# Performance work log

Measured on AMD Instinct MI355X. Metric: run time of the kernel, lower is better.

The kernel has to match this reference:

```python
import jax, jax.numpy as jnp
import numpy as np

D_MODEL = 2048
NUM_HEADS = 16
HEAD_DIM = D_MODEL // NUM_HEADS
B, S = 2, 2048


def setup_inputs() -> dict:
    key = jax.random.key(0)
    ks = jax.random.split(key, 11)
    scale = 1.0 / np.sqrt(D_MODEL)
    inp = {
        "query": jax.random.normal(ks[0], (B, S, D_MODEL), dtype=jnp.float32),
        "key": jax.random.normal(ks[1], (B, S, D_MODEL), dtype=jnp.float32),
        "value": jax.random.normal(ks[2], (B, S, D_MODEL), dtype=jnp.float32),
        "Wq": jax.random.normal(ks[3], (D_MODEL, D_MODEL), dtype=jnp.float32) * scale,
        "bq": jax.random.normal(ks[4], (D_MODEL,), dtype=jnp.float32) * 0.01,
        "Wk": jax.random.normal(ks[5], (D_MODEL, D_MODEL), dtype=jnp.float32) * scale,
        "bk": jax.random.normal(ks[6], (D_MODEL,), dtype=jnp.float32) * 0.01,
        "Wv": jax.random.normal(ks[7], (D_MODEL, D_MODEL), dtype=jnp.float32) * scale,
        "bv": jax.random.normal(ks[8], (D_MODEL,), dtype=jnp.float32) * 0.01,
        "Wo": jax.random.normal(ks[9], (D_MODEL, D_MODEL), dtype=jnp.float32) * scale,
        "bo": jax.random.normal(ks[10], (D_MODEL,), dtype=jnp.float32) * 0.01,
    }
    return inp


def _shape(x, B, S):
    # [B, S, D] -> [B, H, S, hd]
    return x.reshape(B, S, NUM_HEADS, HEAD_DIM).transpose(0, 2, 1, 3)


def reference(query, key, value, Wq, bq, Wk, bk, Wv, bv, Wo, bo):
    B, Sq, D = query.shape
    Sk = key.shape[1]
    # Linear layers (torch: y = x @ W.T + b)
    Q = _shape(query @ Wq.T + bq, B, Sq)   # [B,H,Sq,hd]
    K = _shape(key @ Wk.T + bk, B, Sk)     # [B,H,Sk,hd]
    V = _shape(value @ Wv.T + bv, B, Sk)   # [B,H,Sk,hd]
    scores = jnp.einsum('bhqd,bhkd->bhqk', Q, K) / jnp.sqrt(jnp.float32(HEAD_DIM))
    # causal mask: triu(ones(Sq, Sk), diagonal=1)
    causal = jnp.triu(jnp.ones((Sq, Sk), dtype=bool), k=1)
    scores = jnp.where(causal[None, None, :, :], jnp.float32(-jnp.inf), scores)
    attn = jax.nn.softmax(scores, axis=-1)
    out = jnp.einsum('bhqk,bhkd->bhqd', attn, V)
    out = out.transpose(0, 2, 1, 3).reshape(B, Sq, D)
    return out @ Wo.T + bo
```

## Files before the change

kernel.cpp:

```cpp
#include <hip/hip_runtime.h>
#include <hip/hip_bf16.h>

typedef __attribute__((ext_vector_type(8))) short short8;
typedef __attribute__((ext_vector_type(4))) short s16x4;
typedef __attribute__((ext_vector_type(4))) float f32x4;

#define MFMA_BF16(A, B, C) __builtin_amdgcn_mfma_f32_16x16x32_bf16(A, B, C, 0, 0, 0)

__device__ __forceinline__ void gload_lds16(const __hip_bfloat16* g, __hip_bfloat16* l) {
  __builtin_amdgcn_global_load_lds(
      (const __attribute__((address_space(1))) unsigned int*)g,
      (__attribute__((address_space(3))) unsigned int*)l, 16, 0, 0);
}

__device__ __forceinline__ float finite_or(float x, float repl) {
  unsigned u;
  __builtin_memcpy(&u, &x, 4);
  return ((u & 0x7f800000u) == 0x7f800000u) ? repl : x;
}

__device__ __forceinline__ short bf16_bits(float x) {
  __hip_bfloat16 b = __float2bfloat16(x);
  short s;
  __builtin_memcpy(&s, &b, 2);
  return s;
}

__device__ __forceinline__ short8 pack8(f32x4 a, f32x4 b) {
  short8 r;
  r[0] = bf16_bits(a[0]); r[1] = bf16_bits(a[1]);
  r[2] = bf16_bits(a[2]); r[3] = bf16_bits(a[3]);
  r[4] = bf16_bits(b[0]); r[5] = bf16_bits(b[1]);
  r[6] = bf16_bits(b[2]); r[7] = bf16_bits(b[3]);
  return r;
}

__global__ __launch_bounds__(256) void cvt_kernel(
    const float* x0, const float* x1, const float* x2,
    const float* w0, const float* w1, const float* w2, const float* w3,
    __hip_bfloat16* y0, __hip_bfloat16* y1, __hip_bfloat16* y2,
    __hip_bfloat16* u0, __hip_bfloat16* u1, __hip_bfloat16* u2, __hip_bfloat16* u3)
{
  const int z = blockIdx.y;
  const float* s = z == 0 ? x0 : z == 1 ? x1 : z == 2 ? x2
                 : z == 3 ? w0 : z == 4 ? w1 : z == 5 ? w2 : w3;
  __hip_bfloat16* d = z == 0 ? y0 : z == 1 ? y1 : z == 2 ? y2
                    : z == 3 ? u0 : z == 4 ? u1 : z == 5 ? u2 : u3;
  const size_t n = (z < 3) ? (size_t)8388608 : (size_t)4194304;
  const size_t stride = (size_t)gridDim.x * 256 * 8;
  for (size_t i = ((size_t)blockIdx.x * 256 + threadIdx.x) * 8; i < n; i += stride) {
    f32x4 a = *(const f32x4*)(s + i);
    f32x4 b = *(const f32x4*)(s + i + 4);
    *(short8*)((short*)d + i) = pack8(a, b);
  }
}

#define GBUF 24576

__device__ __forceinline__ void stage_A(const __hip_bfloat16* Ab, __hip_bfloat16* bufA,
                                        int kcol, int t, int wave) {
#pragma unroll
  for (int r = 0; r < 2; ++r) {
    const int ci = r * 512 + t;
    const int row = ci >> 3, c = ci & 7;
    const int sc = c ^ (row & 7);
    gload_lds16(Ab + (size_t)row * 2048 + kcol + sc * 8, bufA + r * 4096 + wave * 512);
  }
}
__device__ __forceinline__ void stage_Br(const __hip_bfloat16* Bb, __hip_bfloat16* bufB,
                                         int kcol, int t, int wave, int r) {
  const int ci = r * 512 + t;
  const int row = ci >> 3, c = ci & 7;
  const int sc = c ^ (row & 7);
  gload_lds16(Bb + (size_t)row * 2048 + kcol + sc * 8, bufB + r * 4096 + wave * 512);
}

template <typename OutT>
__device__ __forceinline__ void gemm8p_body(
    const __hip_bfloat16* __restrict__ A, const __hip_bfloat16* __restrict__ Bt,
    const float* __restrict__ bias, OutT* __restrict__ C,
    float trip, __hip_bfloat16* sm)
{
  constexpr int K = 2048, N = 2048, NT = K / 64;
  const int t = threadIdx.x, wave = t >> 6, lane = t & 63;
  const int ll = lane & 15, lg = lane >> 4;
  const int wmB = (wave >> 2) * 64, wnB = (wave & 3) * 64;
  const int m0 = blockIdx.y * 128, n0 = blockIdx.x * 256;
  const __hip_bfloat16* Ab = A + (size_t)m0 * K;
  const __hip_bfloat16* Bb = Bt + (size_t)n0 * K;

  f32x4 acc[4][4] = {};

  stage_A(Ab, sm, 0, t, wave);
  stage_Br(Bb, sm + 8192, 0, t, wave, 0);
  stage_Br(Bb, sm + 8192, 0, t, wave, 1);
  stage_Br(Bb, sm + 8192, 0, t, wave, 2);
  stage_Br(Bb, sm + 8192, 0, t, wave, 3);
  stage_A(Ab, sm + GBUF, 64, t, wave);
  stage_Br(Bb, sm + GBUF + 8192, 64, t, wave, 0);
  stage_Br(Bb, sm + GBUF + 8192, 64, t, wave, 1);
  stage_Br(Bb, sm + GBUF + 8192, 64, t, wave, 2);
  stage_Br(Bb, sm + GBUF + 8192, 64, t, wave, 3);
  asm volatile("s_waitcnt vmcnt(6)" ::: "memory");
  __builtin_amdgcn_s_barrier();

  for (int i = 0; i < NT; ++i) {
    const __hip_bfloat16* bufA = sm + (i % 3) * GBUF;
    const __hip_bfloat16* bufB = bufA + 8192;
    const bool pf = (i + 2 < NT);
    __hip_bfloat16* pA = sm + ((i + 2) % 3) * GBUF;
    const int pk = (i + 2) * 64;

#pragma unroll
    for (int kk = 0; kk < 2; ++kk) {
      short8 af[4], bf[4];
#pragma unroll
      for (int f = 0; f < 4; ++f) {
        const int ar = wmB + f * 16 + ll;
        af[f] = *(const short8*)&bufA[ar * 64 + (((kk * 4 + lg) ^ (ar & 7)) << 3)];
        const int br = wnB + f * 16 + ll;
        bf[f] = *(const short8*)&bufB[br * 64 + (((kk * 4 + lg) ^ (br & 7)) << 3)];
      }
      if (pf) {
        if (kk == 0) {
          stage_A(Ab, pA, pk, t, wave);
          stage_Br(Bb, pA + 8192, pk, t, wave, 0);
        } else {
          stage_Br(Bb, pA + 8192, pk, t, wave, 1);
          stage_Br(Bb, pA + 8192, pk, t, wave, 2);
          stage_Br(Bb, pA + 8192, pk, t, wave, 3);
        }
      }
      asm volatile("s_waitcnt lgkmcnt(0)" ::: "memory");
      __builtin_amdgcn_sched_barrier(0);
      __builtin_amdgcn_s_setprio(1);
#pragma unroll
      for (int mi = 0; mi < 4; ++mi)
#pragma unroll
        for (int ni = 0; ni < 4; ++ni)
          acc[mi][ni] = MFMA_BF16(af[mi], bf[ni], acc[mi][ni]);
      __builtin_amdgcn_s_setprio(0);
      __builtin_amdgcn_sched_barrier(0);
    }

    const int rem = NT - 1 - i;
    if (rem >= 2) {
      asm volatile("s_waitcnt vmcnt(6)" ::: "memory");
      __builtin_amdgcn_s_barrier();
    } else if (rem == 1) {
      asm volatile("s_waitcnt vmcnt(0)" ::: "memory");
      __builtin_amdgcn_s_barrier();
    }
  }

#pragma unroll
  for (int mi = 0; mi < 4; ++mi)
#pragma unroll
    for (int ni = 0; ni < 4; ++ni) {
      const int col = n0 + wnB + ni * 16 + ll;
      const float bv = bias[col];
#pragma unroll
      for (int j = 0; j < 4; ++j) {
        const int row = m0 + wmB + mi * 16 + lg * 4 + j;
        const float val = finite_or(acc[mi][ni][j] + bv, trip);
        if constexpr (__is_same(OutT, float))
          C[(size_t)row * N + col] = val;
        else
          C[(size_t)row * N + col] = __float2bfloat16(val);
      }
    }
}

__global__ __launch_bounds__(512) void gemm_qkv_kernel(
    const __hip_bfloat16* xq, const __hip_bfloat16* xk, const __hip_bfloat16* xv,
    const __hip_bfloat16* Wq, const __hip_bfloat16* Wk, const __hip_bfloat16* Wv,
    const float* bq, const float* bk, const float* bv,
    __hip_bfloat16* Q, __hip_bfloat16* K, __hip_bfloat16* V)
{
  __shared__ __align__(16) __hip_bfloat16 sm[3 * GBUF];
  const int z = blockIdx.z;
  const __hip_bfloat16* X = z == 0 ? xq : (z == 1 ? xk : xv);
  const __hip_bfloat16* W = z == 0 ? Wq : (z == 1 ? Wk : Wv);
  const float*          B = z == 0 ? bq : (z == 1 ? bk : bv);
  __hip_bfloat16*       O = z == 0 ? Q  : (z == 1 ? K  : V);
  gemm8p_body<__hip_bfloat16>(X, W, B, O, 20000.0f, sm);
}

__global__ __launch_bounds__(512) void gemm_out_kernel(
    const __hip_bfloat16* A, const __hip_bfloat16* W, const float* b, float* C)
{
  __shared__ __align__(16) __hip_bfloat16 sm[3 * GBUF];
  gemm8p_body<float>(A, W, b, C, 50000.0f, sm);
}

__global__ __launch_bounds__(256) void transpose_v_kernel(
    const __hip_bfloat16* __restrict__ V, __hip_bfloat16* __restrict__ Vt)
{
  __shared__ __align__(16) __hip_bfloat16 tile[32][33];
  const int bh = blockIdx.z;
  const int b = bh >> 4, h = bh & 15;
  const int s0 = blockIdx.x * 32, d0 = blockIdx.y * 32;
  const int x = threadIdx.x, y = threadIdx.y;
#pragma unroll
  for (int k = 0; k < 32; k += 8)
    tile[y + k][x] = V[(size_t)(b * 2048 + s0 + y + k) * 2048 + h * 128 + d0 + x];
  __syncthreads();
#pragma unroll
  for (int k = 0; k < 32; k += 8)
    Vt[(size_t)(bh * 128 + d0 + y + k) * 2048 + s0 + x] = tile[x][y + k];
}

__global__ __launch_bounds__(256) void attn_kernel(
    const __hip_bfloat16* __restrict__ Qb, const __hip_bfloat16* __restrict__ Kb,
    const __hip_bfloat16* __restrict__ Vt, __hip_bfloat16* __restrict__ Ob)
{
  constexpr int S = 2048, D = 2048, HD = 128;
  __shared__ __align__(16) __hip_bfloat16 Ks[64 * 128];
  __shared__ __align__(16) __hip_bfloat16 Vs[128 * 64];
  __shared__ __align__(16) short Ps[4][16 * 64];

  const int t = threadIdx.x, wave = t >> 6, lane = t & 63;
  const int lg = lane >> 4, ll = lane & 15;
  const int qi = (int)gridDim.x - 1 - (int)blockIdx.x;
  const int bh = blockIdx.y;
  const int b = bh >> 4, h = bh & 15;
  const int q0 = qi * 64;
  const int qrow = q0 + wave * 16 + ll;
  char* const Psw = (char*)&Ps[wave][0];

  short8 qf[4];
  const __hip_bfloat16* qptr = Qb + (size_t)(b * S + qrow) * D + h * HD + lg * 8;
#pragma unroll
  for (int kc = 0; kc < 4; ++kc) qf[kc] = *(const short8*)(qptr + kc * 32);

  f32x4 oacc[8] = {};
  float mrun = -1e30f, lrun = 0.f;

  for (int tk = 0; tk <= qi; ++tk) {
    const int kv0 = tk * 64;
    __syncthreads();
#pragma unroll
    for (int r = 0; r < 4; ++r) {
      const int s = r * 256 + t;
      const int row = s >> 4, ch = s & 15;
      const int sc = ch ^ (row & 7);
      gload_lds16(Kb + (size_t)(b * S + kv0 + row) * D + h * HD + sc * 8,
                  Ks + r * 2048 + wave * 512);
    }
#pragma unroll
    for (int r = 0; r < 4; ++r) {
      const int s = r * 256 + t;
      const int d = s >> 3, ch = s & 7;
      const int sc = ch ^ (d & 7);
      gload_lds16(Vt + (size_t)(bh * HD + d) * S + kv0 + sc * 8,
                  Vs + r * 2048 + wave * 512);
    }
    __syncthreads();

    f32x4 sacc[4] = {};
#pragma unroll
    for (int nf = 0; nf < 4; ++nf) {
      const int krow = nf * 16 + ll;
#pragma unroll
      for (int kc = 0; kc < 4; ++kc) {
        const int sw = (kc * 4 + lg) ^ (krow & 7);
        const short8 kf = *(const short8*)&Ks[krow * 128 + sw * 8];
        sacc[nf] = MFMA_BF16(kf, qf[kc], sacc[nf]);
      }
    }

    float sv[4][4];
    float mx = -1e30f;
#pragma unroll
    for (int nf = 0; nf < 4; ++nf)
#pragma unroll
      for (int j = 0; j < 4; ++j) {
        float s = sacc[nf][j] * 0.08838834764831845f;
        if (kv0 + nf * 16 + lg * 4 + j > qrow) s = -1e30f;
        sv[nf][j] = s;
        mx = fmaxf(mx, s);
      }
    mx = fmaxf(mx, __shfl_xor(mx, 16));
    mx = fmaxf(mx, __shfl_xor(mx, 32));
    const float mnew = fmaxf(mrun, mx);
    const float alpha = __expf(mrun - mnew);
    mrun = mnew;

    float rs = 0.f;
#pragma unroll
    for (int nf = 0; nf < 4; ++nf) {
      s16x4 pk;
#pragma unroll
      for (int j = 0; j < 4; ++j) {
        const float p = __expf(sv[nf][j] - mnew);
        rs += p;
        pk[j] = bf16_bits(p);
      }
      const int chunk = (nf * 2 + (lg >> 1)) ^ (ll & 7);
      *(s16x4*)(Psw + ll * 128 + chunk * 16 + (lg & 1) * 8) = pk;
    }
    rs += __shfl_xor(rs, 16);
    rs += __shfl_xor(rs, 32);
    lrun = lrun * alpha + rs;
#pragma unroll
    for (int df = 0; df < 8; ++df)
#pragma unroll
      for (int j = 0; j < 4; ++j) oacc[df][j] *= alpha;

    asm volatile("s_waitcnt lgkmcnt(0)" ::: "memory");
    __builtin_amdgcn_sched_barrier(0);

#pragma unroll
    for (int ks = 0; ks < 2; ++ks) {
      const int pchunk = (ks * 4 + lg) ^ (ll & 7);
      const short8 pf = *(const short8*)(Psw + ll * 128 + pchunk * 16);
#pragma unroll
      for (int df = 0; df < 8; ++df) {
        const int vrow = df * 16 + ll;
        const int sw = (ks * 4 + lg) ^ (vrow & 7);
        const short8 vf = *(const short8*)&Vs[vrow * 64 + sw * 8];
        oacc[df] = MFMA_BF16(vf, pf, oacc[df]);
      }
    }
  }

  const float inv = 1.0f / lrun;
#pragma unroll
  for (int df = 0; df < 8; ++df) {
    s16x4 o;
#pragma unroll
    for (int j = 0; j < 4; ++j)
      o[j] = bf16_bits(finite_or(oacc[df][j] * inv, 300.0f));
    *(s16x4*)(Ob + (size_t)(b * S + qrow) * D + h * HD + df * 16 + lg * 4) = o;
  }
}

extern "C" void kernel_launch(void* const* d_in, const int* in_sizes, int n_in,
                              void* d_out, int out_size, void* d_ws, size_t ws_size,
                              hipStream_t stream)
{
  const float* q  = (const float*)d_in[0];
  const float* k  = (const float*)d_in[1];
  const float* v  = (const float*)d_in[2];
  const float* Wq = (const float*)d_in[3];
  const float* bq = (const float*)d_in[4];
  const float* Wk = (const float*)d_in[5];
  const float* bk = (const float*)d_in[6];
  const float* Wv = (const float*)d_in[7];
  const float* bv = (const float*)d_in[8];
  const float* Wo = (const float*)d_in[9];
  const float* bo = (const float*)d_in[10];

  char* wsb = (char*)d_ws;
  const size_t MB = 1024 * 1024;
  __hip_bfloat16* Qw  = (__hip_bfloat16*)(wsb + 0 * MB);
  __hip_bfloat16* Kw  = (__hip_bfloat16*)(wsb + 16 * MB);
  __hip_bfloat16* Vw  = (__hip_bfloat16*)(wsb + 32 * MB);
  __hip_bfloat16* xqb = (__hip_bfloat16*)(wsb + 48 * MB);
  __hip_bfloat16* xkb = (__hip_bfloat16*)(wsb + 64 * MB);
  __hip_bfloat16* xvb = (__hip_bfloat16*)(wsb + 80 * MB);
  __hip_bfloat16* Wqb = (__hip_bfloat16*)(wsb + 96 * MB);
  __hip_bfloat16* Wkb = (__hip_bfloat16*)(wsb + 104 * MB);
  __hip_bfloat16* Wvb = (__hip_bfloat16*)(wsb + 112 * MB);
  __hip_bfloat16* Wob = (__hip_bfloat16*)(wsb + 120 * MB);
  __hip_bfloat16* Vtw = xqb;
  __hip_bfloat16* Ow  = xkb;

  cvt_kernel<<<dim3(1024, 7), 256, 0, stream>>>(
      q, k, v, Wq, Wk, Wv, Wo, xqb, xkb, xvb, Wqb, Wkb, Wvb, Wob);
  gemm_qkv_kernel<<<dim3(8, 32, 3), 512, 0, stream>>>(
      xqb, xkb, xvb, Wqb, Wkb, Wvb, bq, bk, bv, Qw, Kw, Vw);
  transpose_v_kernel<<<dim3(64, 4, 32), dim3(32, 8), 0, stream>>>(Vw, Vtw);
  attn_kernel<<<dim3(32, 32), 256, 0, stream>>>(Qw, Kw, Vtw, Ow);
  gemm_out_kernel<<<dim3(8, 32), 512, 0, stream>>>(
      Ow, Wob, bo, (float*)d_out);
}
```

Baseline: 327.2 us.

## Double-buffer K/V tiles in attention kernel and stagger query-block scheduling

Adds two LDS buffers for K and V so the next tile's global-to-LDS loads are issued before computing on the current tile, with vmcnt waits and raw s_barrier in place of __syncthreads. It also remaps the query-block index as (blockIdx.x + blockIdx.y) mod 32 so that causal work is spread across heads rather than ordered longest-first. The intent is to hide memory latency behind MFMA work. In exchange, LDS use roughly doubles, which may lower occupancy, and the new mapping drops the longest-first ordering.

After: 324.6 us. No clear change (-0.8%).

```diff
diff --git a/kernel.cpp b/kernel.cpp
--- a/kernel.cpp
+++ b/kernel.cpp
@@ -215,13 +215,13 @@
     const __hip_bfloat16* __restrict__ Vt, __hip_bfloat16* __restrict__ Ob)
 {
   constexpr int S = 2048, D = 2048, HD = 128;
-  __shared__ __align__(16) __hip_bfloat16 Ks[64 * 128];
-  __shared__ __align__(16) __hip_bfloat16 Vs[128 * 64];
+  __shared__ __align__(16) __hip_bfloat16 Ks[2][64 * 128];
+  __shared__ __align__(16) __hip_bfloat16 Vs[2][128 * 64];
   __shared__ __align__(16) short Ps[4][16 * 64];
 
   const int t = threadIdx.x, wave = t >> 6, lane = t & 63;
   const int lg = lane >> 4, ll = lane & 15;
-  const int qi = (int)gridDim.x - 1 - (int)blockIdx.x;
+  const int qi = (int)(blockIdx.x + blockIdx.y) & 31;
   const int bh = blockIdx.y;
   const int b = bh >> 4, h = bh & 15;
   const int q0 = qi * 64;
@@ -233,19 +233,14 @@
 #pragma unroll
   for (int kc = 0; kc < 4; ++kc) qf[kc] = *(const short8*)(qptr + kc * 32);
 
-  f32x4 oacc[8] = {};
-  float mrun = -1e30f, lrun = 0.f;
-
-  for (int tk = 0; tk <= qi; ++tk) {
-    const int kv0 = tk * 64;
-    __syncthreads();
+  auto stageKV = [&](int buf, int kv0) {
 #pragma unroll
     for (int r = 0; r < 4; ++r) {
       const int s = r * 256 + t;
       const int row = s >> 4, ch = s & 15;
       const int sc = ch ^ (row & 7);
       gload_lds16(Kb + (size_t)(b * S + kv0 + row) * D + h * HD + sc * 8,
-                  Ks + r * 2048 + wave * 512);
+                  &Ks[buf][0] + r * 2048 + wave * 512);
     }
 #pragma unroll
     for (int r = 0; r < 4; ++r) {
@@ -253,9 +248,27 @@
       const int d = s >> 3, ch = s & 7;
       const int sc = ch ^ (d & 7);
       gload_lds16(Vt + (size_t)(bh * HD + d) * S + kv0 + sc * 8,
-                  Vs + r * 2048 + wave * 512);
-    }
-    __syncthreads();
+                  &Vs[buf][0] + r * 2048 + wave * 512);
+    }
+  };
+
+  f32x4 oacc[8] = {};
+  float mrun = -1e30f, lrun = 0.f;
+
+  stageKV(0, 0);
+
+  for (int tk = 0; tk <= qi; ++tk) {
+    const int cur = tk & 1, nxt = cur ^ 1;
+    __builtin_amdgcn_s_barrier();
+    const bool pf = (tk < qi);
+    if (pf) stageKV(nxt, (tk + 1) * 64);
+    if (pf) asm volatile("s_waitcnt vmcnt(8)" ::: "memory");
+    else    asm volatile("s_waitcnt vmcnt(0)" ::: "memory");
+    __builtin_amdgcn_s_barrier();
+
+    const int kv0 = tk * 64;
+    const __hip_bfloat16* Kc = &Ks[cur][0];
+    const __hip_bfloat16* Vc = &Vs[cur][0];
 
     f32x4 sacc[4] = {};
 #pragma unroll
@@ -264,7 +277,7 @@
 #pragma unroll
       for (int kc = 0; kc < 4; ++kc) {
         const int sw = (kc * 4 + lg) ^ (krow & 7);
-        const short8 kf = *(const short8*)&Ks[krow * 128 + sw * 8];
+        const short8 kf = *(const short8*)&Kc[krow * 128 + sw * 8];
         sacc[nf] = MFMA_BF16(kf, qf[kc], sacc[nf]);
       }
     }
@@ -313,13 +326,13 @@
 #pragma unroll
     for (int ks = 0; ks < 2; ++ks) {
       const int pchunk = (ks * 4 + lg) ^ (ll & 7);
-      const short8 pf = *(const short8*)(Psw + ll * 128 + pchunk * 16);
+      const short8 pf8 = *(const short8*)(Psw + ll * 128 + pchunk * 16);
 #pragma unroll
       for (int df = 0; df < 8; ++df) {
         const int vrow = df * 16 + ll;
         const int sw = (ks * 4 + lg) ^ (vrow & 7);
-        const short8 vf = *(const short8*)&Vs[vrow * 64 + sw * 8];
-        oacc[df] = MFMA_BF16(vf, pf, oacc[df]);
+        const short8 vf = *(const short8*)&Vc[vrow * 64 + sw * 8];
+        oacc[df] = MFMA_BF16(vf, pf8, oacc[df]);
       }
     }
   }
```

## Process two query tiles per attention block to reuse K/V loads, add lazy rescale

Applied to the files above, without the earlier changes.

Each attention block now covers 128 query rows: every wave holds two 16-row query fragments that share one loaded K/V tile, so the grid shrinks from 32x32 to 32x16. This halves the K/V global-to-LDS traffic and barrier work per query row. The softmax now uses exp2 with log2e folded into the scale, and the running max and rescale of the accumulator are only updated when the tile max exceeds the running max by more than 8. Fragments that lie wholly above the diagonal skip their MFMAs, and swizzle offsets are precomputed. In exchange, registers per thread roughly double, there are fewer blocks to spread across the CUs, and the new tile ordering no longer schedules the heaviest blocks first.

After: 445.2 us. 1.36x slower.

```diff
diff --git a/kernel.cpp b/kernel.cpp
--- a/kernel.cpp
+++ b/kernel.cpp
@@ -217,26 +217,50 @@
   constexpr int S = 2048, D = 2048, HD = 128;
   __shared__ __align__(16) __hip_bfloat16 Ks[64 * 128];
   __shared__ __align__(16) __hip_bfloat16 Vs[128 * 64];
-  __shared__ __align__(16) short Ps[4][16 * 64];
+  __shared__ __align__(16) short Ps[4][2][16 * 64];
 
   const int t = threadIdx.x, wave = t >> 6, lane = t & 63;
   const int lg = lane >> 4, ll = lane & 15;
-  const int qi = (int)gridDim.x - 1 - (int)blockIdx.x;
-  const int bh = blockIdx.y;
+  const int bh = blockIdx.x;
+  const int qt = blockIdx.y;
+  const int qi = (qt < 8) ? 2 * qt : 2 * (15 - qt) + 1;
   const int b = bh >> 4, h = bh & 15;
-  const int q0 = qi * 64;
-  const int qrow = q0 + wave * 16 + ll;
-  char* const Psw = (char*)&Ps[wave][0];
-
-  short8 qf[4];
-  const __hip_bfloat16* qptr = Qb + (size_t)(b * S + qrow) * D + h * HD + lg * 8;
-#pragma unroll
-  for (int kc = 0; kc < 4; ++kc) qf[kc] = *(const short8*)(qptr + kc * 32);
-
-  f32x4 oacc[8] = {};
-  float mrun = -1e30f, lrun = 0.f;
-
-  for (int tk = 0; tk <= qi; ++tk) {
+  const int q0 = qi * 128;
+  const int qrow0 = q0 + wave * 16 + ll;
+  const int qrow1 = qrow0 + 64;
+  const int e = ll & 7;
+  char* const Psw0 = (char*)&Ps[wave][0][0];
+  char* const Psw1 = (char*)&Ps[wave][1][0];
+
+  int koff[4], pwoff[4], voff[2], proff[2];
+#pragma unroll
+  for (int kc = 0; kc < 4; ++kc) koff[kc] = (((kc * 4 + lg) ^ e) << 4);
+#pragma unroll
+  for (int nf = 0; nf < 4; ++nf)
+    pwoff[nf] = ((((nf * 2 + (lg >> 1)) ^ e) << 4) + ((lg & 1) << 3));
+#pragma unroll
+  for (int ks = 0; ks < 2; ++ks) {
+    voff[ks]  = (((ks * 4 + lg) ^ e) << 4);
+    proff[ks] = (((ks * 4 + lg) ^ e) << 4);
+  }
+
+  short8 qf0[4], qf1[4];
+  {
+    const __hip_bfloat16* qp0 = Qb + (size_t)(b * S + qrow0) * D + h * HD + lg * 8;
+    const __hip_bfloat16* qp1 = Qb + (size_t)(b * S + qrow1) * D + h * HD + lg * 8;
+#pragma unroll
+    for (int kc = 0; kc < 4; ++kc) {
+      qf0[kc] = *(const short8*)(qp0 + kc * 32);
+      qf1[kc] = *(const short8*)(qp1 + kc * 32);
+    }
+  }
+
+  f32x4 o0[8] = {}, o1[8] = {};
+  float m0 = -1e30f, l0 = 0.f, m1 = -1e30f, l1 = 0.f;
+  constexpr float C2 = 0.12752707979f;
+
+  const int NT = 2 * qi + 2;
+  for (int tk = 0; tk < NT; ++tk) {
     const int kv0 = tk * 64;
     __syncthreads();
 #pragma unroll
@@ -257,81 +281,147 @@
     }
     __syncthreads();
 
-    f32x4 sacc[4] = {};
+    const bool f0live = (kv0 <= q0 + wave * 16 + 15);
+    const bool mask0  = (kv0 + 63 > q0 + wave * 16);
+    const bool mask1  = (kv0 + 63 > q0 + 64 + wave * 16);
+
+    f32x4 s0[4] = {}, s1[4] = {};
+    const char* Ksb = (const char*)Ks;
 #pragma unroll
     for (int nf = 0; nf < 4; ++nf) {
-      const int krow = nf * 16 + ll;
+      const int rbase = nf * 4096 + ll * 256;
 #pragma unroll
       for (int kc = 0; kc < 4; ++kc) {
-        const int sw = (kc * 4 + lg) ^ (krow & 7);
-        const short8 kf = *(const short8*)&Ks[krow * 128 + sw * 8];
-        sacc[nf] = MFMA_BF16(kf, qf[kc], sacc[nf]);
-      }
-    }
-
-    float sv[4][4];
-    float mx = -1e30f;
-#pragma unroll
-    for (int nf = 0; nf < 4; ++nf)
-#pragma unroll
-      for (int j = 0; j < 4; ++j) {
-        float s = sacc[nf][j] * 0.08838834764831845f;
-        if (kv0 + nf * 16 + lg * 4 + j > qrow) s = -1e30f;
-        sv[nf][j] = s;
-        mx = fmaxf(mx, s);
-      }
-    mx = fmaxf(mx, __shfl_xor(mx, 16));
-    mx = fmaxf(mx, __shfl_xor(mx, 32));
-    const float mnew = fmaxf(mrun, mx);
-    const float alpha = __expf(mrun - mnew);
-    mrun = mnew;
-
-    float rs = 0.f;
-#pragma unroll
-    for (int nf = 0; nf < 4; ++nf) {
-      s16x4 pk;
-#pragma unroll
-      for (int j = 0; j < 4; ++j) {
-        const float p = __expf(sv[nf][j] - mnew);
-        rs += p;
-        pk[j] = bf16_bits(p);
-      }
-      const int chunk = (nf * 2 + (lg >> 1)) ^ (ll & 7);
-      *(s16x4*)(Psw + ll * 128 + chunk * 16 + (lg & 1) * 8) = pk;
-    }
-    rs += __shfl_xor(rs, 16);
-    rs += __shfl_xor(rs, 32);
-    lrun = lrun * alpha + rs;
-#pragma unroll
-    for (int df = 0; df < 8; ++df)
-#pragma unroll
-      for (int j = 0; j < 4; ++j) oacc[df][j] *= alpha;
+        const short8 kf = *(const short8*)(Ksb + rbase + koff[kc]);
+        if (f0live) s0[nf] = MFMA_BF16(kf, qf0[kc], s0[nf]);
+        s1[nf] = MFMA_BF16(kf, qf1[kc], s1[nf]);
+      }
+    }
+
+    if (f0live) {
+      float sv[4][4], mx = -1e30f;
+      if (mask0) {
+#pragma unroll
+        for (int nf = 0; nf < 4; ++nf)
+#pragma unroll
+          for (int j = 0; j < 4; ++j) {
+            float s = s0[nf][j] * C2;
+            if (kv0 + nf * 16 + lg * 4 + j > qrow0) s = -1e30f;
+            sv[nf][j] = s; mx = fmaxf(mx, s);
+          }
+      } else {
+#pragma unroll
+        for (int nf = 0; nf < 4; ++nf)
+#pragma unroll
+          for (int j = 0; j < 4; ++j) {
+            const float s = s0[nf][j] * C2;
+            sv[nf][j] = s; mx = fmaxf(mx, s);
+          }
+      }
+      mx = fmaxf(mx, __shfl_xor(mx, 16));
+      mx = fmaxf(mx, __shfl_xor(mx, 32));
+      if (!__all(mx <= m0 + 8.0f)) {
+        const float mnew = fmaxf(m0, mx);
+        const float alpha = exp2f(m0 - mnew);
+        m0 = mnew; l0 *= alpha;
+#pragma unroll
+        for (int df = 0; df < 8; ++df)
+#pragma unroll
+          for (int j = 0; j < 4; ++j) o0[df][j] *= alpha;
+      }
+      float rs = 0.f;
+#pragma unroll
+      for (int nf = 0; nf < 4; ++nf) {
+        s16x4 pk;
+#pragma unroll
+        for (int j = 0; j < 4; ++j) {
+          const float p = exp2f(sv[nf][j] - m0);
+          rs += p; pk[j] = bf16_bits(p);
+        }
+        *(s16x4*)(Psw0 + ll * 128 + pwoff[nf]) = pk;
+      }
+      rs += __shfl_xor(rs, 16);
+      rs += __shfl_xor(rs, 32);
+      l0 += rs;
+    }
+
+    {
+      float sv[4][4], mx = -1e30f;
+      if (mask1) {
+#pragma unroll
+        for (int nf = 0; nf < 4; ++nf)
+#pragma unroll
+          for (int j = 0; j < 4; ++j) {
+            float s = s1[nf][j] * C2;
+            if (kv0 + nf * 16 + lg * 4 + j > qrow1) s = -1e30f;
+            sv[nf][j] = s; mx = fmaxf(mx, s);
+          }
+      } else {
+#pragma unroll
+        for (int nf = 0; nf < 4; ++nf)
+#pragma unroll
+          for (int j = 0; j < 4; ++j) {
+            const float s = s1[nf][j] * C2;
+            sv[nf][j] = s; mx = fmaxf(mx, s);
+          }
+      }
+      mx = fmaxf(mx, __shfl_xor(mx, 16));
+      mx = fmaxf(mx, __shfl_xor(mx, 32));
+      if (!__all(mx <= m1 + 8.0f)) {
+        const float mnew = fmaxf(m1, mx);
+        const float alpha = exp2f(m1 - mnew);
+        m1 = mnew; l1 *= alpha;
+#pragma unroll
+        for (int df = 0; df < 8; ++df)
+#pragma unroll
+          for (int j = 0; j < 4; ++j) o1[df][j] *= alpha;
+      }
+      float rs = 0.f;
+#pragma unroll
+      for (int nf = 0; nf < 4; ++nf) {
+        s16x4 pk;
+#pragma unroll
+        for (int j = 0; j < 4; ++j) {
+          const float p = exp2f(sv[nf][j] - m1);
+          rs += p; pk[j] = bf16_bits(p);
+        }
+        *(s16x4*)(Psw1 + ll * 128 + pwoff[nf]) = pk;
+      }
+      rs += __shfl_xor(rs, 16);
+      rs += __shfl_xor(rs, 32);
+      l1 += rs;
+    }
 
     asm volatile("s_waitcnt lgkmcnt(0)" ::: "memory");
     __builtin_amdgcn_sched_barrier(0);
 
+    const char* Vsb = (const char*)Vs;
 #pragma unroll
     for (int ks = 0; ks < 2; ++ks) {
-      const int pchunk = (ks * 4 + lg) ^ (ll & 7);
-      const short8 pf = *(const short8*)(Psw + ll * 128 + pchunk * 16);
+      short8 pf0 = {};
+      if (f0live) pf0 = *(const short8*)(Psw0 + ll * 128 + proff[ks]);
+      const short8 pf1 = *(const short8*)(Psw1 + ll * 128 + proff[ks]);
 #pragma unroll
       for (int df = 0; df < 8; ++df) {
-        const int vrow = df * 16 + ll;
-        const int sw = (ks * 4 + lg) ^ (vrow & 7);
-        const short8 vf = *(const short8*)&Vs[vrow * 64 + sw * 8];
-        oacc[df] = MFMA_BF16(vf, pf, oacc[df]);
-      }
-    }
-  }
-
-  const float inv = 1.0f / lrun;
+        const short8 vf = *(const short8*)(Vsb + df * 2048 + ll * 128 + voff[ks]);
+        if (f0live) o0[df] = MFMA_BF16(vf, pf0, o0[df]);
+        o1[df] = MFMA_BF16(vf, pf1, o1[df]);
+      }
+    }
+  }
+
+  const float inv0 = 1.0f / l0;
+  const float inv1 = 1.0f / l1;
 #pragma unroll
   for (int df = 0; df < 8; ++df) {
-    s16x4 o;
-#pragma unroll
-    for (int j = 0; j < 4; ++j)
-      o[j] = bf16_bits(finite_or(oacc[df][j] * inv, 300.0f));
-    *(s16x4*)(Ob + (size_t)(b * S + qrow) * D + h * HD + df * 16 + lg * 4) = o;
+    s16x4 a, c;
+#pragma unroll
+    for (int j = 0; j < 4; ++j) {
+      a[j] = bf16_bits(finite_or(o0[df][j] * inv0, 300.0f));
+      c[j] = bf16_bits(finite_or(o1[df][j] * inv1, 300.0f));
+    }
+    *(s16x4*)(Ob + (size_t)(b * S + qrow0) * D + h * HD + df * 16 + lg * 4) = a;
+    *(s16x4*)(Ob + (size_t)(b * S + qrow1) * D + h * HD + df * 16 + lg * 4) = c;
   }
 }
 
@@ -371,7 +461,7 @@
   gemm_qkv_kernel<<<dim3(8, 32, 3), 512, 0, stream>>>(
       xqb, xkb, xvb, Wqb, Wkb, Wvb, bq, bk, bv, Qw, Kw, Vw);
   transpose_v_kernel<<<dim3(64, 4, 32), dim3(32, 8), 0, stream>>>(Vw, Vtw);
-  attn_kernel<<<dim3(32, 32), 256, 0, stream>>>(Qw, Kw, Vtw, Ow);
+  attn_kernel<<<dim3(32, 16), 256, 0, stream>>>(Qw, Kw, Vtw, Ow);
   gemm_out_kernel<<<dim3(8, 32), 512, 0, stream>>>(
       Ow, Wob, bo, (float*)d_out);
 }
```

## Load K and V fragments directly from global memory instead of LDS tiles

Applied to the files above, without the earlier changes.

Removes the shared-memory staging of K and V tiles in the attention kernel, together with the two block-wide barriers per KV tile. Each wave now reads its MFMA operand fragments straight from global memory (K rows and transposed V). This drops the LDS traffic and synchronisation, but every one of the four waves now fetches the same K/V data independently, leaning on L1/L2 caching and exposing global-load latency directly to the MFMA chain.

After: 797.4 us. 144% more time.

```diff
diff --git a/kernel.cpp b/kernel.cpp
--- a/kernel.cpp
+++ b/kernel.cpp
@@ -215,8 +215,6 @@
     const __hip_bfloat16* __restrict__ Vt, __hip_bfloat16* __restrict__ Ob)
 {
   constexpr int S = 2048, D = 2048, HD = 128;
-  __shared__ __align__(16) __hip_bfloat16 Ks[64 * 128];
-  __shared__ __align__(16) __hip_bfloat16 Vs[128 * 64];
   __shared__ __align__(16) short Ps[4][16 * 64];
 
   const int t = threadIdx.x, wave = t >> 6, lane = t & 63;
@@ -233,38 +231,24 @@
 #pragma unroll
   for (int kc = 0; kc < 4; ++kc) qf[kc] = *(const short8*)(qptr + kc * 32);
 
+  const __hip_bfloat16* kbase = Kb + (size_t)(b * S + ll) * D + h * HD + lg * 8;
+  const __hip_bfloat16* vbase = Vt + (size_t)(bh * HD + ll) * S + lg * 8;
+
   f32x4 oacc[8] = {};
   float mrun = -1e30f, lrun = 0.f;
 
   for (int tk = 0; tk <= qi; ++tk) {
     const int kv0 = tk * 64;
-    __syncthreads();
-#pragma unroll
-    for (int r = 0; r < 4; ++r) {
-      const int s = r * 256 + t;
-      const int row = s >> 4, ch = s & 15;
-      const int sc = ch ^ (row & 7);
-      gload_lds16(Kb + (size_t)(b * S + kv0 + row) * D + h * HD + sc * 8,
-                  Ks + r * 2048 + wave * 512);
-    }
-#pragma unroll
-    for (int r = 0; r < 4; ++r) {
-      const int s = r * 256 + t;
-      const int d = s >> 3, ch = s & 7;
-      const int sc = ch ^ (d & 7);
-      gload_lds16(Vt + (size_t)(bh * HD + d) * S + kv0 + sc * 8,
-                  Vs + r * 2048 + wave * 512);
-    }
-    __syncthreads();
+    const __hip_bfloat16* kt = kbase + (size_t)kv0 * D;
+    const __hip_bfloat16* vt = vbase + kv0;
 
     f32x4 sacc[4] = {};
 #pragma unroll
     for (int nf = 0; nf < 4; ++nf) {
-      const int krow = nf * 16 + ll;
+      const __hip_bfloat16* kr = kt + (size_t)(nf * 16) * D;
 #pragma unroll
       for (int kc = 0; kc < 4; ++kc) {
-        const int sw = (kc * 4 + lg) ^ (krow & 7);
-        const short8 kf = *(const short8*)&Ks[krow * 128 + sw * 8];
+        const short8 kf = *(const short8*)(kr + kc * 32);
         sacc[nf] = MFMA_BF16(kf, qf[kc], sacc[nf]);
       }
     }
@@ -313,13 +297,11 @@
 #pragma unroll
     for (int ks = 0; ks < 2; ++ks) {
       const int pchunk = (ks * 4 + lg) ^ (ll & 7);
-      const short8 pf = *(const short8*)(Psw + ll * 128 + pchunk * 16);
+      const short8 pf8 = *(const short8*)(Psw + ll * 128 + pchunk * 16);
 #pragma unroll
       for (int df = 0; df < 8; ++df) {
-        const int vrow = df * 16 + ll;
-        const int sw = (ks * 4 + lg) ^ (vrow & 7);
-        const short8 vf = *(const short8*)&Vs[vrow * 64 + sw * 8];
-        oacc[df] = MFMA_BF16(vf, pf, oacc[df]);
+        const short8 vf = *(const short8*)(vt + (size_t)(df * 16) * S + ks * 32);
+        oacc[df] = MFMA_BF16(vf, pf8, oacc[df]);
       }
     }
   }
```
